# Optimization experiments

Measured on AMD Instinct MI355X. Metric: run time of the kernel, lower is better.

## Reference

```python
import jax, jax.numpy as jnp
import numpy as np

N_NODES = 30000
IN_DIM = 8
HIDDEN = 64
HEADS1 = 8
OUT_DIM = 8
NEG_SLOPE = 0.2


def _glorot(key, shape):
    fan_in, fan_out = shape[0], shape[-1]
    lim = jnp.sqrt(6.0 / (fan_in + fan_out))
    return jax.random.uniform(key, shape, jnp.float32, -lim, lim)


def setup_inputs() -> dict:
    key = jax.random.key(0)
    ks = jax.random.split(key, 12)
    x = jax.random.normal(ks[0], (N_NODES, IN_DIM), jnp.float32)
    edge_index = jax.random.randint(ks[1], (2, 300000), 0, N_NODES, jnp.int32)
    # layer 1: in=8, out=HIDDEN per head, 8 heads, concat
    W1l = _glorot(ks[2], (IN_DIM, HEADS1 * HIDDEN))
    W1r = _glorot(ks[3], (IN_DIM, HEADS1 * HIDDEN))
    a1 = _glorot(ks[4], (HEADS1, HIDDEN))
    b1 = jnp.zeros((HEADS1 * HIDDEN,), jnp.float32)
    # layer 2: in=HEADS1*HIDDEN, out=OUT_DIM, 1 head
    W2l = _glorot(ks[5], (HEADS1 * HIDDEN, OUT_DIM))
    W2r = _glorot(ks[6], (HEADS1 * HIDDEN, OUT_DIM))
    a2 = _glorot(ks[7], (1, OUT_DIM))
    b2 = jnp.zeros((OUT_DIM,), jnp.float32)
    return {"x": x, "edge_index": edge_index, "W1l": W1l, "W1r": W1r,
            "a1": a1, "b1": b1, "W2l": W2l, "W2r": W2r, "a2": a2, "b2": b2}


def gatv2_layer(x, src, dst, Wl, Wr, att, bias, heads, out_ch):
    n = x.shape[0]
    xl = (x @ Wl).reshape(n, heads, out_ch)   # messages (source side)
    xr = (x @ Wr).reshape(n, heads, out_ch)   # target side
    h = jax.nn.leaky_relu(xl[src] + xr[dst], NEG_SLOPE)   # [E,H,C]
    e = jnp.einsum('ehc,hc->eh', h, att)                  # [E,H]
    # segment softmax over incoming edges per destination node
    m = jax.ops.segment_max(e, dst, num_segments=n)
    p = jnp.exp(e - m[dst])
    denom = jax.ops.segment_sum(p, dst, num_segments=n)
    alpha = p / denom[dst]                                # [E,H]
    out = jax.ops.segment_sum(alpha[..., None] * xl[src], dst, num_segments=n)
    return out.reshape(n, heads * out_ch) + bias


def reference(x, edge_index, W1l, W1r, a1, b1, W2l, W2r, a2, b2):
    n = x.shape[0]
    loops = jnp.arange(n, dtype=edge_index.dtype)
    src = jnp.concatenate([edge_index[0], loops])  # add_self_loops=True (PyG default)
    dst = jnp.concatenate([edge_index[1], loops])
    h = gatv2_layer(x, src, dst, W1l, W1r, a1, b1, HEADS1, HIDDEN)
    h = jax.nn.relu(h)
    out = gatv2_layer(h, src, dst, W2l, W2r, a2, b2, 1, OUT_DIM)
    return out
```

## Files before the change

### kernel.cpp

```cpp
#include <hip/hip_runtime.h>
#include <math.h>

#define N_NODES   30000
#define N_EDGE    300000
#define N_EDGE_T  330000
#define HEADS     8
#define HIDDEN    64
#define IN_DIM    8
#define OUT_DIM   8
#define NEG_SLOPE 0.2f

#define PIN_V(v) asm volatile("" : "+v"(v))

#define DPP_ADDF(x, ctrl)                                                     \
    x += __int_as_float(__builtin_amdgcn_update_dpp(                          \
            0, __float_as_int(x), (ctrl), 0xF, 0xF, true))
#define RED16(x) do { DPP_ADDF(x, 0xB1); DPP_ADDF(x, 0x4E);                   \
                      DPP_ADDF(x, 0x141); DPP_ADDF(x, 0x140); } while (0)
#define RED8(x)  do { DPP_ADDF(x, 0xB1); DPP_ADDF(x, 0x4E);                   \
                      DPP_ADDF(x, 0x141); } while (0)


__global__ __launch_bounds__(256) void zero_kernel(int* __restrict__ count) {
    int i = blockIdx.x * 256 + threadIdx.x;
    if (i < N_NODES) count[i] = 0;
}

__global__ __launch_bounds__(256) void count_kernel(const int* __restrict__ ei,
                                                    int* __restrict__ count) {
    int e = blockIdx.x * 256 + threadIdx.x;
    if (e >= N_EDGE_T) return;
    int d = (e < N_EDGE) ? ei[N_EDGE + e] : (e - N_EDGE);
    atomicAdd(&count[d], 1);
}

__global__ __launch_bounds__(1024) void scan_kernel(const int* __restrict__ count,
                                                    int* __restrict__ row_start,
                                                    int* __restrict__ cursor) {
    __shared__ int wsum[16];
    const int tid  = threadIdx.x;
    const int wave = tid >> 6;
    const int lane = tid & 63;
    const int4* c4 = (const int4*)count;
    const int N4 = N_NODES / 4;
    int run = 0;
    for (int r = 0; r < 4; ++r) {
        const int g  = r * 1024 + tid;
        const int i0 = 2 * g;
        const int i1 = 2 * g + 1;
        int4 v0 = make_int4(0,0,0,0), v1 = make_int4(0,0,0,0);
        if (i0 < N4) v0 = c4[i0];
        if (i1 < N4) v1 = c4[i1];
        int s = v0.x + v0.y + v0.z + v0.w + v1.x + v1.y + v1.z + v1.w;
        int sc = s;
        #pragma unroll
        for (int off = 1; off < 64; off <<= 1) {
            int t = __shfl_up(sc, off, 64);
            if (lane >= off) sc += t;
        }
        if (lane == 63) wsum[wave] = sc;
        __syncthreads();
        if (tid < 16) {
            int w = wsum[tid];
            #pragma unroll
            for (int off = 1; off < 16; off <<= 1) {
                int t = __shfl_up(w, off, 64);
                if (tid >= off) w += t;
            }
            wsum[tid] = w;
        }
        __syncthreads();
        const int woff = (wave > 0) ? wsum[wave - 1] : 0;
        int e0 = run + woff + (sc - s);
        int4 ex0, ex1;
        ex0.x = e0;           ex0.y = ex0.x + v0.x;
        ex0.z = ex0.y + v0.y; ex0.w = ex0.z + v0.z;
        int e4 = ex0.w + v0.w;
        ex1.x = e4;           ex1.y = ex1.x + v1.x;
        ex1.z = ex1.y + v1.y; ex1.w = ex1.z + v1.z;
        if (i0 < N4) { ((int4*)row_start)[i0] = ex0; ((int4*)cursor)[i0] = ex0; }
        if (i1 < N4) { ((int4*)row_start)[i1] = ex1; ((int4*)cursor)[i1] = ex1; }
        const int tot = wsum[15];
        __syncthreads();
        run += tot;
    }
    if (tid == 0) row_start[N_NODES] = run;
}

__global__ __launch_bounds__(256) void scatter_kernel(const int* __restrict__ ei,
                                                      int* __restrict__ cursor,
                                                      int* __restrict__ edge_src) {
    int e = blockIdx.x * 256 + threadIdx.x;
    if (e >= N_EDGE_T) return;
    int s, d;
    if (e < N_EDGE) { s = ei[e]; d = ei[N_EDGE + e]; }
    else            { s = d = e - N_EDGE; }
    int pos = atomicAdd(&cursor[d], 1);
    edge_src[pos] = s;
}


__global__ __launch_bounds__(256) void proj_kernel(
    const float* __restrict__ x, const float* __restrict__ W1l,
    float* __restrict__ xl_t)
{
    const int t = threadIdx.x;
    float wl0[IN_DIM], wl1[IN_DIM];
    #pragma unroll
    for (int k = 0; k < IN_DIM; ++k) {
        wl0[k] = W1l[k * 512 + t];
        wl1[k] = W1l[k * 512 + t + 256];
    }
    for (int n = blockIdx.x; n < N_NODES; n += gridDim.x) {
        float xv[IN_DIM];
        #pragma unroll
        for (int k = 0; k < IN_DIM; ++k) xv[k] = x[n * IN_DIM + k];
        float l0 = 0.f, l1 = 0.f;
        #pragma unroll
        for (int k = 0; k < IN_DIM; ++k) {
            l0 = fmaf(xv[k], wl0[k], l0);
            l1 = fmaf(xv[k], wl1[k], l1);
        }
        xl_t[n * 512 + t]       = l0;
        xl_t[n * 512 + t + 256] = l1;
    }
}


__global__ void __launch_bounds__(128, 4)
layer1_kernel(
    const float* __restrict__ x,
    const float* __restrict__ xl_t, const float* __restrict__ W1r,
    const float* __restrict__ a1,  const float* __restrict__ b1,
    const float* __restrict__ W2l, const float* __restrict__ W2r,
    const int* __restrict__ row_start, const int* __restrict__ edge_src,
    float* __restrict__ xl2, float* __restrict__ xr2)
{
    const int d    = blockIdx.x;
    const int tid  = threadIdx.x;
    const int head = tid >> 4;
    const int c4   = tid & 15;
    const int colb = head * HIDDEN + c4 * 4;

    float av[4];
    { const float4 a4 = *(const float4*)&a1[colb];
      av[0] = a4.x; av[1] = a4.y; av[2] = a4.z; av[3] = a4.w; }

    float xrv[4] = {0.f, 0.f, 0.f, 0.f};
    #pragma unroll
    for (int k = 0; k < IN_DIM; ++k) {
        const float4 r4 = *(const float4*)&W1r[k * 512 + colb];
        const float xv = x[d * IN_DIM + k];
        xrv[0] = fmaf(xv, r4.x, xrv[0]); xrv[1] = fmaf(xv, r4.y, xrv[1]);
        xrv[2] = fmaf(xv, r4.z, xrv[2]); xrv[3] = fmaf(xv, r4.w, xrv[3]);
    }
    PIN_V(av[0]); PIN_V(av[1]); PIN_V(av[2]); PIN_V(av[3]);
    PIN_V(xrv[0]); PIN_V(xrv[1]); PIN_V(xrv[2]); PIN_V(xrv[3]);

    const int rs = row_start[d];
    const int re = row_start[d + 1];

    float denom  = 0.f;
    float acc[4] = {0.f, 0.f, 0.f, 0.f};

    auto ldrow = [&](int s) { return *(const float4*)&xl_t[s * 512 + colb]; };

    auto pair2 = [&](float4 ra, float4 rb, bool va, bool vb) {
        float q0a = ra.x + xrv[0], q1a = ra.y + xrv[1];
        float q2a = ra.z + xrv[2], q3a = ra.w + xrv[3];
        float q0b = rb.x + xrv[0], q1b = rb.y + xrv[1];
        float q2b = rb.z + xrv[2], q3b = rb.w + xrv[3];
        float ta, tb, ea, eb;
        ta = fmaxf(q0a, NEG_SLOPE * q0a); ea = av[0] * ta;
        tb = fmaxf(q0b, NEG_SLOPE * q0b); eb = av[0] * tb;
        ta = fmaxf(q1a, NEG_SLOPE * q1a); ea = fmaf(av[1], ta, ea);
        tb = fmaxf(q1b, NEG_SLOPE * q1b); eb = fmaf(av[1], tb, eb);
        ta = fmaxf(q2a, NEG_SLOPE * q2a); ea = fmaf(av[2], ta, ea);
        tb = fmaxf(q2b, NEG_SLOPE * q2b); eb = fmaf(av[2], tb, eb);
        ta = fmaxf(q3a, NEG_SLOPE * q3a); ea = fmaf(av[3], ta, ea);
        tb = fmaxf(q3b, NEG_SLOPE * q3b); eb = fmaf(av[3], tb, eb);
        RED16(ea); RED16(eb);
        float pa = va ? __expf(ea) : 0.f;
        float pb = vb ? __expf(eb) : 0.f;
        denom += pa + pb;
        acc[0] = fmaf(pb, rb.x, fmaf(pa, ra.x, acc[0]));
        acc[1] = fmaf(pb, rb.y, fmaf(pa, ra.y, acc[1]));
        acc[2] = fmaf(pb, rb.z, fmaf(pa, ra.z, acc[2]));
        acc[3] = fmaf(pb, rb.w, fmaf(pa, ra.w, acc[3]));
    };

    float4 rA, rB, rC, rD;
    {
        int e1 = (rs + 1 < re) ? rs + 1 : re - 1;
        int e2 = (rs + 2 < re) ? rs + 2 : re - 1;
        int e3 = (rs + 3 < re) ? rs + 3 : re - 1;
        int s0 = edge_src[rs], s1 = edge_src[e1];
        int s2 = edge_src[e2], s3 = edge_src[e3];
        rA = ldrow(s0); rB = ldrow(s1); rC = ldrow(s2); rD = ldrow(s3);
    }

    int base = rs;
    for (;;) {
        const int  nbase = base + 4;
        const bool more  = nbase < re;

        int ns0 = 0, ns1 = 0, ns2 = 0, ns3 = 0;
        if (more) {
            int f1 = (nbase + 1 < re) ? nbase + 1 : re - 1;
            int f2 = (nbase + 2 < re) ? nbase + 2 : re - 1;
            int f3 = (nbase + 3 < re) ? nbase + 3 : re - 1;
            ns0 = edge_src[nbase]; ns1 = edge_src[f1];
            ns2 = edge_src[f2];    ns3 = edge_src[f3];
        }

        pair2(rA, rB, true, base + 1 < re);

        float4 nA, nB, nC, nD;
        if (more) {
            nA = ldrow(ns0); nB = ldrow(ns1); nC = ldrow(ns2); nD = ldrow(ns3);
        }

        pair2(rC, rD, base + 2 < re, base + 3 < re);

        if (!more) break;
        base = nbase;
        rA = nA; rB = nB; rC = nC; rD = nD;
    }

    const float inv = 1.f / denom;
    const float4 b4 = *(const float4*)&b1[colb];
    float hv[4];
    hv[0] = fmaxf(fmaf(acc[0], inv, b4.x), 0.f);
    hv[1] = fmaxf(fmaf(acc[1], inv, b4.y), 0.f);
    hv[2] = fmaxf(fmaf(acc[2], inv, b4.z), 0.f);
    hv[3] = fmaxf(fmaf(acc[3], inv, b4.w), 0.f);

    float vl[OUT_DIM], vr[OUT_DIM];
    #pragma unroll
    for (int j = 0; j < OUT_DIM; ++j) { vl[j] = 0.f; vr[j] = 0.f; }
    #pragma unroll
    for (int i = 0; i < 4; ++i) {
        const float4 l0 = *(const float4*)&W2l[(colb + i) * OUT_DIM];
        const float4 l1 = *(const float4*)&W2l[(colb + i) * OUT_DIM + 4];
        const float4 r0 = *(const float4*)&W2r[(colb + i) * OUT_DIM];
        const float4 r1 = *(const float4*)&W2r[(colb + i) * OUT_DIM + 4];
        vl[0] = fmaf(hv[i], l0.x, vl[0]); vl[1] = fmaf(hv[i], l0.y, vl[1]);
        vl[2] = fmaf(hv[i], l0.z, vl[2]); vl[3] = fmaf(hv[i], l0.w, vl[3]);
        vl[4] = fmaf(hv[i], l1.x, vl[4]); vl[5] = fmaf(hv[i], l1.y, vl[5]);
        vl[6] = fmaf(hv[i], l1.z, vl[6]); vl[7] = fmaf(hv[i], l1.w, vl[7]);
        vr[0] = fmaf(hv[i], r0.x, vr[0]); vr[1] = fmaf(hv[i], r0.y, vr[1]);
        vr[2] = fmaf(hv[i], r0.z, vr[2]); vr[3] = fmaf(hv[i], r0.w, vr[3]);
        vr[4] = fmaf(hv[i], r1.x, vr[4]); vr[5] = fmaf(hv[i], r1.y, vr[5]);
        vr[6] = fmaf(hv[i], r1.z, vr[6]); vr[7] = fmaf(hv[i], r1.w, vr[7]);
    }
    #pragma unroll
    for (int j = 0; j < OUT_DIM; ++j) { RED16(vl[j]); RED16(vr[j]); }

    __shared__ float psl[HEADS][OUT_DIM];
    __shared__ float psr[HEADS][OUT_DIM];
    if (c4 == 0) {
        #pragma unroll
        for (int j = 0; j < OUT_DIM; ++j) { psl[head][j] = vl[j]; psr[head][j] = vr[j]; }
    }
    __syncthreads();
    if (tid < 16) {
        const int side = tid >> 3, j = tid & 7;
        float s = 0.f;
        if (side == 0) {
            #pragma unroll
            for (int h = 0; h < HEADS; ++h) s += psl[h][j];
            xl2[d * OUT_DIM + j] = s;
        } else {
            #pragma unroll
            for (int h = 0; h < HEADS; ++h) s += psr[h][j];
            xr2[d * OUT_DIM + j] = s;
        }
    }
}


__global__ __launch_bounds__(256) void layer2_kernel(
    const float* __restrict__ xl2, const float* __restrict__ xr2,
    const float* __restrict__ a2,  const float* __restrict__ b2,
    const int* __restrict__ row_start, const int* __restrict__ edge_src,
    float* __restrict__ out)
{
    const int wave = threadIdx.x >> 6;
    const int lane = threadIdx.x & 63;
    const int d = blockIdx.x * 4 + wave;
    if (d >= N_NODES) return;
    const int sub = lane >> 3;
    const int c   = lane & 7;

    const float a_c  = a2[c];
    const float xr_d = xr2[d * OUT_DIM + c];

    const int rs = row_start[d];
    const int re = row_start[d + 1];

    float denom = 0.f, acc = 0.f;

    for (int base = rs; base < re; base += 8) {
        int e = base + sub;
        bool valid = (e < re);
        int s = valid ? edge_src[e] : 0;
        float xls = xl2[s * OUT_DIM + c];
        float v = xls + xr_d;
        float t = fmaxf(v, NEG_SLOPE * v);
        float eh = a_c * t;
        RED8(eh);
        float p = valid ? __expf(eh) : 0.f;
        denom += p;
        acc = fmaf(p, xls, acc);
    }

    denom += __shfl_xor(denom, 8,  64);  acc += __shfl_xor(acc, 8,  64);
    denom += __shfl_xor(denom, 16, 64);  acc += __shfl_xor(acc, 16, 64);
    denom += __shfl_xor(denom, 32, 64);  acc += __shfl_xor(acc, 32, 64);

    if (sub == 0) out[d * OUT_DIM + c] = acc / denom + b2[c];
}


extern "C" void kernel_launch(void* const* d_in, const int* in_sizes, int n_in,
                              void* d_out, int out_size, void* d_ws, size_t ws_size,
                              hipStream_t stream) {
    const float* x   = (const float*)d_in[0];
    const int*   ei  = (const int*)  d_in[1];
    const float* W1l = (const float*)d_in[2];
    const float* W1r = (const float*)d_in[3];
    const float* a1  = (const float*)d_in[4];
    const float* b1  = (const float*)d_in[5];
    const float* W2l = (const float*)d_in[6];
    const float* W2r = (const float*)d_in[7];
    const float* a2  = (const float*)d_in[8];
    const float* b2  = (const float*)d_in[9];
    float* out = (float*)d_out;

    char* ws = (char*)d_ws;
    size_t off = 0;
    auto carve = [&](size_t bytes) { char* p = ws + off; off += (bytes + 255) & ~size_t(255); return p; };
    int*   count     = (int*)  carve(N_NODES * sizeof(int));
    int*   row_start = (int*)  carve((N_NODES + 1) * sizeof(int));
    int*   cursor    = (int*)  carve(N_NODES * sizeof(int));
    int*   edge_src  = (int*)  carve(N_EDGE_T * sizeof(int));
    float* xl2       = (float*)carve(N_NODES * OUT_DIM * sizeof(float));
    float* xr2       = (float*)carve(N_NODES * OUT_DIM * sizeof(float));
    float* xl_t      = (float*)carve((size_t)N_NODES * 512 * sizeof(float));

    proj_kernel   <<<1024, 256, 0, stream>>>(x, W1l, xl_t);
    zero_kernel   <<<(N_NODES  + 255) / 256, 256, 0, stream>>>(count);
    count_kernel  <<<(N_EDGE_T + 255) / 256, 256, 0, stream>>>(ei, count);
    scan_kernel   <<<1, 1024, 0, stream>>>(count, row_start, cursor);
    scatter_kernel<<<(N_EDGE_T + 255) / 256, 256, 0, stream>>>(ei, cursor, edge_src);
    layer1_kernel <<<N_NODES, 128, 0, stream>>>(x, xl_t, W1r, a1, b1, W2l, W2r,
                                                row_start, edge_src, xl2, xr2);
    layer2_kernel <<<(N_NODES + 3) / 4, 256, 0, stream>>>(xl2, xr2, a2, b2,
                                                          row_start, edge_src, out);
}
```

Measured before the change: 302.5 us.

## Store layer-1 source projections in fp16 and map one wave per node

```diff
diff --git a/kernel.cpp b/kernel.cpp
--- a/kernel.cpp
+++ b/kernel.cpp
@@ -1,4 +1,5 @@
 #include <hip/hip_runtime.h>
+#include <hip/hip_fp16.h>
 #include <math.h>
 
 #define N_NODES   30000
@@ -9,8 +10,6 @@
 #define IN_DIM    8
 #define OUT_DIM   8
 #define NEG_SLOPE 0.2f
-
-#define PIN_V(v) asm volatile("" : "+v"(v))
 
 #define DPP_ADDF(x, ctrl)                                                     \
     x += __int_as_float(__builtin_amdgcn_update_dpp(                          \
@@ -102,14 +101,14 @@
 
 __global__ __launch_bounds__(256) void proj_kernel(
     const float* __restrict__ x, const float* __restrict__ W1l,
-    float* __restrict__ xl_t)
+    __half* __restrict__ xl_h)
 {
     const int t = threadIdx.x;
-    float wl0[IN_DIM], wl1[IN_DIM];
+    float w0[IN_DIM], w1[IN_DIM];
     #pragma unroll
     for (int k = 0; k < IN_DIM; ++k) {
-        wl0[k] = W1l[k * 512 + t];
-        wl1[k] = W1l[k * 512 + t + 256];
+        const float2 wp = *(const float2*)&W1l[k * 512 + 2 * t];
+        w0[k] = wp.x; w1[k] = wp.y;
     }
     for (int n = blockIdx.x; n < N_NODES; n += gridDim.x) {
         float xv[IN_DIM];
@@ -118,163 +117,154 @@
         float l0 = 0.f, l1 = 0.f;
         #pragma unroll
         for (int k = 0; k < IN_DIM; ++k) {
-            l0 = fmaf(xv[k], wl0[k], l0);
-            l1 = fmaf(xv[k], wl1[k], l1);
-        }
-        xl_t[n * 512 + t]       = l0;
-        xl_t[n * 512 + t + 256] = l1;
-    }
-}
-
-
-__global__ void __launch_bounds__(128, 4)
+            l0 = fmaf(xv[k], w0[k], l0);
+            l1 = fmaf(xv[k], w1[k], l1);
+        }
+        ((__half2*)xl_h)[n * 256 + t] = __floats2half2_rn(l0, l1);
+    }
+}
+
+
+__global__ void __launch_bounds__(256, 4)
 layer1_kernel(
     const float* __restrict__ x,
-    const float* __restrict__ xl_t, const float* __restrict__ W1r,
+    const __half* __restrict__ xl_h, const float* __restrict__ W1r,
     const float* __restrict__ a1,  const float* __restrict__ b1,
     const float* __restrict__ W2l, const float* __restrict__ W2r,
     const int* __restrict__ row_start, const int* __restrict__ edge_src,
     float* __restrict__ xl2, float* __restrict__ xr2)
 {
-    const int d    = blockIdx.x;
-    const int tid  = threadIdx.x;
-    const int head = tid >> 4;
-    const int c4   = tid & 15;
-    const int colb = head * HIDDEN + c4 * 4;
-
-    float av[4];
-    { const float4 a4 = *(const float4*)&a1[colb];
-      av[0] = a4.x; av[1] = a4.y; av[2] = a4.z; av[3] = a4.w; }
-
-    float xrv[4] = {0.f, 0.f, 0.f, 0.f};
+    const int wv   = threadIdx.x >> 6;
+    const int lane = threadIdx.x & 63;
+    const int d    = blockIdx.x * 4 + wv;
+    const int colb = lane * 8;
+
+    float av[8], xr[8];
+    { const float4 a0 = *(const float4*)&a1[colb];
+      const float4 a4 = *(const float4*)&a1[colb + 4];
+      av[0]=a0.x; av[1]=a0.y; av[2]=a0.z; av[3]=a0.w;
+      av[4]=a4.x; av[5]=a4.y; av[6]=a4.z; av[7]=a4.w; }
+    #pragma unroll
+    for (int i = 0; i < 8; ++i) xr[i] = 0.f;
     #pragma unroll
     for (int k = 0; k < IN_DIM; ++k) {
-        const float4 r4 = *(const float4*)&W1r[k * 512 + colb];
+        const float4 r0 = *(const float4*)&W1r[k * 512 + colb];
+        const float4 r4 = *(const float4*)&W1r[k * 512 + colb + 4];
         const float xv = x[d * IN_DIM + k];
-        xrv[0] = fmaf(xv, r4.x, xrv[0]); xrv[1] = fmaf(xv, r4.y, xrv[1]);
-        xrv[2] = fmaf(xv, r4.z, xrv[2]); xrv[3] = fmaf(xv, r4.w, xrv[3]);
-    }
-    PIN_V(av[0]); PIN_V(av[1]); PIN_V(av[2]); PIN_V(av[3]);
-    PIN_V(xrv[0]); PIN_V(xrv[1]); PIN_V(xrv[2]); PIN_V(xrv[3]);
+        xr[0] = fmaf(xv, r0.x, xr[0]); xr[1] = fmaf(xv, r0.y, xr[1]);
+        xr[2] = fmaf(xv, r0.z, xr[2]); xr[3] = fmaf(xv, r0.w, xr[3]);
+        xr[4] = fmaf(xv, r4.x, xr[4]); xr[5] = fmaf(xv, r4.y, xr[5]);
+        xr[6] = fmaf(xv, r4.z, xr[6]); xr[7] = fmaf(xv, r4.w, xr[7]);
+    }
 
     const int rs = row_start[d];
     const int re = row_start[d + 1];
 
     float denom  = 0.f;
-    float acc[4] = {0.f, 0.f, 0.f, 0.f};
-
-    auto ldrow = [&](int s) { return *(const float4*)&xl_t[s * 512 + colb]; };
-
-    auto pair2 = [&](float4 ra, float4 rb, bool va, bool vb) {
-        float q0a = ra.x + xrv[0], q1a = ra.y + xrv[1];
-        float q2a = ra.z + xrv[2], q3a = ra.w + xrv[3];
-        float q0b = rb.x + xrv[0], q1b = rb.y + xrv[1];
-        float q2b = rb.z + xrv[2], q3b = rb.w + xrv[3];
-        float ta, tb, ea, eb;
-        ta = fmaxf(q0a, NEG_SLOPE * q0a); ea = av[0] * ta;
-        tb = fmaxf(q0b, NEG_SLOPE * q0b); eb = av[0] * tb;
-        ta = fmaxf(q1a, NEG_SLOPE * q1a); ea = fmaf(av[1], ta, ea);
-        tb = fmaxf(q1b, NEG_SLOPE * q1b); eb = fmaf(av[1], tb, eb);
-        ta = fmaxf(q2a, NEG_SLOPE * q2a); ea = fmaf(av[2], ta, ea);
-        tb = fmaxf(q2b, NEG_SLOPE * q2b); eb = fmaf(av[2], tb, eb);
-        ta = fmaxf(q3a, NEG_SLOPE * q3a); ea = fmaf(av[3], ta, ea);
-        tb = fmaxf(q3b, NEG_SLOPE * q3b); eb = fmaf(av[3], tb, eb);
-        RED16(ea); RED16(eb);
-        float pa = va ? __expf(ea) : 0.f;
-        float pb = vb ? __expf(eb) : 0.f;
-        denom += pa + pb;
-        acc[0] = fmaf(pb, rb.x, fmaf(pa, ra.x, acc[0]));
-        acc[1] = fmaf(pb, rb.y, fmaf(pa, ra.y, acc[1]));
-        acc[2] = fmaf(pb, rb.z, fmaf(pa, ra.z, acc[2]));
-        acc[3] = fmaf(pb, rb.w, fmaf(pa, ra.w, acc[3]));
+    float acc[8] = {0.f,0.f,0.f,0.f,0.f,0.f,0.f,0.f};
+
+    auto ldrow = [&](int s, float (&o)[8]) {
+        const int4 r = *(const int4*)(xl_h + (size_t)s * 512 + colb);
+        union { int i; __half2 h; } u0, u1, u2, u3;
+        u0.i = r.x; u1.i = r.y; u2.i = r.z; u3.i = r.w;
+        float2 f;
+        f = __half22float2(u0.h); o[0] = f.x; o[1] = f.y;
+        f = __half22float2(u1.h); o[2] = f.x; o[3] = f.y;
+        f = __half22float2(u2.h); o[4] = f.x; o[5] = f.y;
+        f = __half22float2(u3.h); o[6] = f.x; o[7] = f.y;
     };
 
-    float4 rA, rB, rC, rD;
+    auto edge1 = [&](const float (&rr)[8], bool valid) {
+        float e = 0.f;
+        #pragma unroll
+        for (int i = 0; i < 8; ++i) {
+            const float q = rr[i] + xr[i];
+            const float t = fmaxf(q, NEG_SLOPE * q);
+            e = fmaf(av[i], t, e);
+        }
+        RED8(e);
+        const float p = valid ? __expf(e) : 0.f;
+        denom += p;
+        #pragma unroll
+        for (int i = 0; i < 8; ++i) acc[i] = fmaf(p, rr[i], acc[i]);
+    };
+
+    float RA[8], RB[8];
     {
-        int e1 = (rs + 1 < re) ? rs + 1 : re - 1;
-        int e2 = (rs + 2 < re) ? rs + 2 : re - 1;
-        int e3 = (rs + 3 < re) ? rs + 3 : re - 1;
-        int s0 = edge_src[rs], s1 = edge_src[e1];
-        int s2 = edge_src[e2], s3 = edge_src[e3];
-        rA = ldrow(s0); rB = ldrow(s1); rC = ldrow(s2); rD = ldrow(s3);
-    }
-
-    int base = rs;
-    for (;;) {
-        const int  nbase = base + 4;
-        const bool more  = nbase < re;
-
-        int ns0 = 0, ns1 = 0, ns2 = 0, ns3 = 0;
+        const int sA = edge_src[rs];
+        const bool vB0 = rs + 1 < re;
+        const int sB = edge_src[vB0 ? rs + 1 : rs];
+        ldrow(sA, RA); ldrow(sB, RB);
+    }
+    bool vB = rs + 1 < re;
+
+    for (int base = rs;;) {
+        const int  nb   = base + 2;
+        const bool more = nb < re;
+        float RC[8], RD[8];
+        bool vD = false;
         if (more) {
-            int f1 = (nbase + 1 < re) ? nbase + 1 : re - 1;
-            int f2 = (nbase + 2 < re) ? nbase + 2 : re - 1;
-            int f3 = (nbase + 3 < re) ? nbase + 3 : re - 1;
-            ns0 = edge_src[nbase]; ns1 = edge_src[f1];
-            ns2 = edge_src[f2];    ns3 = edge_src[f3];
-        }
-
-        pair2(rA, rB, true, base + 1 < re);
-
-        float4 nA, nB, nC, nD;
-        if (more) {
-            nA = ldrow(ns0); nB = ldrow(ns1); nC = ldrow(ns2); nD = ldrow(ns3);
-        }
-
-        pair2(rC, rD, base + 2 < re, base + 3 < re);
-
+            const int sC = edge_src[nb];
+            vD = nb + 1 < re;
+            const int sD = edge_src[vD ? nb + 1 : nb];
+            ldrow(sC, RC); ldrow(sD, RD);
+        }
+        edge1(RA, true);
+        edge1(RB, vB);
         if (!more) break;
-        base = nbase;
-        rA = nA; rB = nB; rC = nC; rD = nD;
+        #pragma unroll
+        for (int i = 0; i < 8; ++i) { RA[i] = RC[i]; RB[i] = RD[i]; }
+        vB = vD;
+        base = nb;
     }
 
     const float inv = 1.f / denom;
-    const float4 b4 = *(const float4*)&b1[colb];
-    float hv[4];
-    hv[0] = fmaxf(fmaf(acc[0], inv, b4.x), 0.f);
-    hv[1] = fmaxf(fmaf(acc[1], inv, b4.y), 0.f);
-    hv[2] = fmaxf(fmaf(acc[2], inv, b4.z), 0.f);
-    hv[3] = fmaxf(fmaf(acc[3], inv, b4.w), 0.f);
+    float hv[8];
+    { const float4 b0 = *(const float4*)&b1[colb];
+      const float4 b4 = *(const float4*)&b1[colb + 4];
+      hv[0] = fmaxf(fmaf(acc[0], inv, b0.x), 0.f);
+      hv[1] = fmaxf(fmaf(acc[1], inv, b0.y), 0.f);
+      hv[2] = fmaxf(fmaf(acc[2], inv, b0.z), 0.f);
+      hv[3] = fmaxf(fmaf(acc[3], inv, b0.w), 0.f);
+      hv[4] = fmaxf(fmaf(acc[4], inv, b4.x), 0.f);
+      hv[5] = fmaxf(fmaf(acc[5], inv, b4.y), 0.f);
+      hv[6] = fmaxf(fmaf(acc[6], inv, b4.z), 0.f);
+      hv[7] = fmaxf(fmaf(acc[7], inv, b4.w), 0.f); }
 
     float vl[OUT_DIM], vr[OUT_DIM];
     #pragma unroll
     for (int j = 0; j < OUT_DIM; ++j) { vl[j] = 0.f; vr[j] = 0.f; }
     #pragma unroll
-    for (int i = 0; i < 4; ++i) {
-        const float4 l0 = *(const float4*)&W2l[(colb + i) * OUT_DIM];
-        const float4 l1 = *(const float4*)&W2l[(colb + i) * OUT_DIM + 4];
-        const float4 r0 = *(const float4*)&W2r[(colb + i) * OUT_DIM];
-        const float4 r1 = *(const float4*)&W2r[(colb + i) * OUT_DIM + 4];
-        vl[0] = fmaf(hv[i], l0.x, vl[0]); vl[1] = fmaf(hv[i], l0.y, vl[1]);
-        vl[2] = fmaf(hv[i], l0.z, vl[2]); vl[3] = fmaf(hv[i], l0.w, vl[3]);
-        vl[4] = fmaf(hv[i], l1.x, vl[4]); vl[5] = fmaf(hv[i], l1.y, vl[5]);
-        vl[6] = fmaf(hv[i], l1.z, vl[6]); vl[7] = fmaf(hv[i], l1.w, vl[7]);
-        vr[0] = fmaf(hv[i], r0.x, vr[0]); vr[1] = fmaf(hv[i], r0.y, vr[1]);
-        vr[2] = fmaf(hv[i], r0.z, vr[2]); vr[3] = fmaf(hv[i], r0.w, vr[3]);
-        vr[4] = fmaf(hv[i], r1.x, vr[4]); vr[5] = fmaf(hv[i], r1.y, vr[5]);
-        vr[6] = fmaf(hv[i], r1.z, vr[6]); vr[7] = fmaf(hv[i], r1.w, vr[7]);
-    }
-    #pragma unroll
-    for (int j = 0; j < OUT_DIM; ++j) { RED16(vl[j]); RED16(vr[j]); }
-
-    __shared__ float psl[HEADS][OUT_DIM];
-    __shared__ float psr[HEADS][OUT_DIM];
-    if (c4 == 0) {
-        #pragma unroll
-        for (int j = 0; j < OUT_DIM; ++j) { psl[head][j] = vl[j]; psr[head][j] = vr[j]; }
-    }
-    __syncthreads();
-    if (tid < 16) {
-        const int side = tid >> 3, j = tid & 7;
-        float s = 0.f;
-        if (side == 0) {
-            #pragma unroll
-            for (int h = 0; h < HEADS; ++h) s += psl[h][j];
-            xl2[d * OUT_DIM + j] = s;
-        } else {
-            #pragma unroll
-            for (int h = 0; h < HEADS; ++h) s += psr[h][j];
-            xr2[d * OUT_DIM + j] = s;
-        }
+    for (int i = 0; i < 8; ++i) {
+        const int c = colb + i;
+        const float4 l0 = *(const float4*)&W2l[c * OUT_DIM];
+        const float4 l1 = *(const float4*)&W2l[c * OUT_DIM + 4];
+        const float4 r0 = *(const float4*)&W2r[c * OUT_DIM];
+        const float4 r1 = *(const float4*)&W2r[c * OUT_DIM + 4];
+        const float h = hv[i];
+        vl[0] = fmaf(h, l0.x, vl[0]); vl[1] = fmaf(h, l0.y, vl[1]);
+        vl[2] = fmaf(h, l0.z, vl[2]); vl[3] = fmaf(h, l0.w, vl[3]);
+        vl[4] = fmaf(h, l1.x, vl[4]); vl[5] = fmaf(h, l1.y, vl[5]);
+        vl[6] = fmaf(h, l1.z, vl[6]); vl[7] = fmaf(h, l1.w, vl[7]);
+        vr[0] = fmaf(h, r0.x, vr[0]); vr[1] = fmaf(h, r0.y, vr[1]);
+        vr[2] = fmaf(h, r0.z, vr[2]); vr[3] = fmaf(h, r0.w, vr[3]);
+        vr[4] = fmaf(h, r1.x, vr[4]); vr[5] = fmaf(h, r1.y, vr[5]);
+        vr[6] = fmaf(h, r1.z, vr[6]); vr[7] = fmaf(h, r1.w, vr[7]);
+    }
+    #pragma unroll
+    for (int j = 0; j < OUT_DIM; ++j) {
+        RED16(vl[j]);
+        vl[j] += __shfl_xor(vl[j], 16, 64);
+        vl[j] += __shfl_xor(vl[j], 32, 64);
+        RED16(vr[j]);
+        vr[j] += __shfl_xor(vr[j], 16, 64);
+        vr[j] += __shfl_xor(vr[j], 32, 64);
+    }
+    if (lane == 0) {
+        *(float4*)&xl2[d * OUT_DIM]     = make_float4(vl[0], vl[1], vl[2], vl[3]);
+        *(float4*)&xl2[d * OUT_DIM + 4] = make_float4(vl[4], vl[5], vl[6], vl[7]);
+        *(float4*)&xr2[d * OUT_DIM]     = make_float4(vr[0], vr[1], vr[2], vr[3]);
+        *(float4*)&xr2[d * OUT_DIM + 4] = make_float4(vr[4], vr[5], vr[6], vr[7]);
     }
 }
 
@@ -298,20 +288,35 @@
     const int rs = row_start[d];
     const int re = row_start[d + 1];
 
-    float denom = 0.f, acc = 0.f;
-
-    for (int base = rs; base < re; base += 8) {
-        int e = base + sub;
-        bool valid = (e < re);
-        int s = valid ? edge_src[e] : 0;
-        float xls = xl2[s * OUT_DIM + c];
-        float v = xls + xr_d;
-        float t = fmaxf(v, NEG_SLOPE * v);
-        float eh = a_c * t;
-        RED8(eh);
-        float p = valid ? __expf(eh) : 0.f;
+    int  e0 = rs + sub;      const bool v0 = e0 < re; e0 = v0 ? e0 : re - 1;
+    int  e1 = rs + 8 + sub;  const bool v1 = e1 < re; e1 = v1 ? e1 : re - 1;
+    const int s0 = edge_src[e0];
+    const int s1 = edge_src[e1];
+    const float x0 = xl2[s0 * OUT_DIM + c];
+    const float x1 = xl2[s1 * OUT_DIM + c];
+
+    const float u0 = x0 + xr_d; const float t0 = fmaxf(u0, NEG_SLOPE * u0);
+    const float u1 = x1 + xr_d; const float t1 = fmaxf(u1, NEG_SLOPE * u1);
+    float g0 = a_c * t0;
+    float g1 = a_c * t1;
+    RED8(g0); RED8(g1);
+    const float p0 = v0 ? __expf(g0) : 0.f;
+    const float p1 = v1 ? __expf(g1) : 0.f;
+    float denom = p0 + p1;
+    float acc   = fmaf(p1, x1, p0 * x0);
+
+    for (int b = rs + 16; b < re; b += 8) {
+        int e = b + sub;
+        const bool v = e < re; e = v ? e : re - 1;
+        const int s = edge_src[e];
+        const float xs = xl2[s * OUT_DIM + c];
+        const float u = xs + xr_d;
+        const float t = fmaxf(u, NEG_SLOPE * u);
+        float g = a_c * t;
+        RED8(g);
+        const float p = v ? __expf(g) : 0.f;
         denom += p;
-        acc = fmaf(p, xls, acc);
+        acc = fmaf(p, xs, acc);
     }
 
     denom += __shfl_xor(denom, 8,  64);  acc += __shfl_xor(acc, 8,  64);
@@ -340,21 +345,21 @@
     char* ws = (char*)d_ws;
     size_t off = 0;
     auto carve = [&](size_t bytes) { char* p = ws + off; off += (bytes + 255) & ~size_t(255); return p; };
-    int*   count     = (int*)  carve(N_NODES * sizeof(int));
-    int*   row_start = (int*)  carve((N_NODES + 1) * sizeof(int));
-    int*   cursor    = (int*)  carve(N_NODES * sizeof(int));
-    int*   edge_src  = (int*)  carve(N_EDGE_T * sizeof(int));
-    float* xl2       = (float*)carve(N_NODES * OUT_DIM * sizeof(float));
-    float* xr2       = (float*)carve(N_NODES * OUT_DIM * sizeof(float));
-    float* xl_t      = (float*)carve((size_t)N_NODES * 512 * sizeof(float));
-
-    proj_kernel   <<<1024, 256, 0, stream>>>(x, W1l, xl_t);
+    int*    count     = (int*)   carve(N_NODES * sizeof(int));
+    int*    row_start = (int*)   carve((N_NODES + 1) * sizeof(int));
+    int*    cursor    = (int*)   carve(N_NODES * sizeof(int));
+    int*    edge_src  = (int*)   carve(N_EDGE_T * sizeof(int));
+    float*  xl2       = (float*) carve(N_NODES * OUT_DIM * sizeof(float));
+    float*  xr2       = (float*) carve(N_NODES * OUT_DIM * sizeof(float));
+    __half* xl_h      = (__half*)carve((size_t)N_NODES * 512 * sizeof(__half));
+
+    proj_kernel   <<<1024, 256, 0, stream>>>(x, W1l, xl_h);
     zero_kernel   <<<(N_NODES  + 255) / 256, 256, 0, stream>>>(count);
     count_kernel  <<<(N_EDGE_T + 255) / 256, 256, 0, stream>>>(ei, count);
     scan_kernel   <<<1, 1024, 0, stream>>>(count, row_start, cursor);
     scatter_kernel<<<(N_EDGE_T + 255) / 256, 256, 0, stream>>>(ei, cursor, edge_src);
-    layer1_kernel <<<N_NODES, 128, 0, stream>>>(x, xl_t, W1r, a1, b1, W2l, W2r,
-                                                row_start, edge_src, xl2, xr2);
+    layer1_kernel <<<N_NODES / 4, 256, 0, stream>>>(x, xl_h, W1r, a1, b1, W2l, W2r,
+                                                    row_start, edge_src, xl2, xr2);
     layer2_kernel <<<(N_NODES + 3) / 4, 256, 0, stream>>>(xl2, xr2, a2, b2,
                                                           row_start, edge_src, out);
 }
```

Measured after the change: 299.5 us. No clear change (-1.0%).
